# Optimization experiments

Measured on AMD Instinct MI355X. Metric: run time of the kernel, lower is better.

Reference implementation:

```python
import jax, jax.numpy as jnp
import numpy as np

EMB = 1024
HEADS = 16
HEAD_DIM = EMB // HEADS

def setup_inputs() -> dict:
    key = jax.random.key(0)
    ks = jax.random.split(key, 12)
    s = 0.02
    x = jax.random.normal(ks[0], (2, 2048, EMB), dtype=jnp.float32)
    return {
        "x": x,
        "wq": jax.random.normal(ks[1], (EMB, EMB), jnp.float32) * s,
        "bq": jnp.zeros((EMB,), jnp.float32),
        "wk": jax.random.normal(ks[2], (EMB, EMB), jnp.float32) * s,
        "bk": jnp.zeros((EMB,), jnp.float32),
        "wv": jax.random.normal(ks[3], (EMB, EMB), jnp.float32) * s,
        "bv": jnp.zeros((EMB,), jnp.float32),
        "wo": jax.random.normal(ks[4], (EMB, EMB), jnp.float32) * s,
        "bo": jnp.zeros((EMB,), jnp.float32),
        "gamma": jnp.ones((EMB,), jnp.float32),
        "beta": jnp.zeros((EMB,), jnp.float32),
    }

def _layernorm(x, gamma, beta, eps=1e-5):
    mu = jnp.mean(x, axis=-1, keepdims=True)
    var = jnp.mean(jnp.square(x - mu), axis=-1, keepdims=True)
    return (x - mu) * jax.lax.rsqrt(var + eps) * gamma + beta

def reference(x, wq, bq, wk, bk, wv, bv, wo, bo, gamma, beta):
    B, T, D = x.shape
    H, d_k = HEADS, HEAD_DIM
    # Linear(y = x W^T + b), then split heads
    q = (x @ wq.T + bq).reshape(B, T, H, d_k)
    k = (x @ wk.T + bk).reshape(B, T, H, d_k)
    v = (x @ wv.T + bv).reshape(B, T, H, d_k)
    scores = jnp.einsum('bthd,bshd->bhts', q, k) / jnp.sqrt(jnp.float32(d_k))
    attn = jax.nn.softmax(scores, axis=-1)  # dropout is identity in eval mode
    out = jnp.einsum('bhts,bshd->bthd', attn, v).reshape(B, T, D)
    out = out @ wo.T + bo
    return _layernorm(x + out, gamma, beta)
```

## Files before the change

### kernel.cpp

```cpp
#include <hip/hip_runtime.h>
#include <stdint.h>
#include <stddef.h>


typedef __bf16 bf16_t;
typedef bf16_t bf16x8 __attribute__((ext_vector_type(8)));
typedef float f32x16 __attribute__((ext_vector_type(16)));
typedef float f32x2 __attribute__((ext_vector_type(2)));
typedef uint16_t u16x8 __attribute__((ext_vector_type(8)));

#define MFMA32(a, b, c) __builtin_amdgcn_mfma_f32_32x32x16_bf16((a), (b), (c), 0, 0, 0)

__device__ __forceinline__ uint16_t f2bf(float f) {
  __bf16 h = (__bf16)f;
  return *(uint16_t*)&h;
}

__device__ __forceinline__ void gload16(const void* g, void* l) {
  __builtin_amdgcn_global_load_lds((const __attribute__((address_space(1))) void*)g,
                                   (__attribute__((address_space(3))) void*)l,
                                   16, 0, 0);
}

__global__ __launch_bounds__(256) void cvt_all(
    const float* __restrict__ x, const float* __restrict__ wq,
    const float* __restrict__ wk, const float* __restrict__ wv,
    const float* __restrict__ wo, uint16_t* __restrict__ xb,
    uint16_t* __restrict__ wqb, uint16_t* __restrict__ wkb,
    uint16_t* __restrict__ wvb, uint16_t* __restrict__ wob) {
  const int gid = blockIdx.x * 256 + threadIdx.x;
  const float* src; uint16_t* dst; int off;
  if (gid < 1048576) {
    src = x; dst = xb; off = gid;
  } else {
    const int t = gid - 1048576;
    off = t & 262143;
    switch (t >> 18) {
      case 0: src = wq; dst = wqb; break;
      case 1: src = wk; dst = wkb; break;
      case 2: src = wv; dst = wvb; break;
      default: src = wo; dst = wob; break;
    }
  }
  const float4 f = ((const float4*)src)[off];
  uint64_t p = (uint64_t)f2bf(f.x) | ((uint64_t)f2bf(f.y) << 16) |
               ((uint64_t)f2bf(f.z) << 32) | ((uint64_t)f2bf(f.w) << 48);
  ((uint64_t*)dst)[off] = p;
}

template <int MODE>
__device__ __forceinline__ void gemm128(uint16_t* __restrict__ smem,
                                        const uint16_t* __restrict__ A,
                                        const uint16_t* __restrict__ Bt,
                                        const float* __restrict__ bias,
                                        float oscale,
                                        uint16_t* __restrict__ outb,
                                        int m0, int n0) {
  uint16_t* sAp = smem;
  uint16_t* sBp = smem + 8192;
  const int tid = threadIdx.x;
  const int lane = tid & 63, w = tid >> 6;
  const int l31 = lane & 31, half = lane >> 5;
  const int wm = (w >> 1) * 64, wn = (w & 1) * 64;

  const int ch0 = tid, ch1 = tid + 256;
  const int r0 = ch0 >> 2, g0 = (((ch0 & 3) ^ (r0 & 3)) << 3);
  const int r1 = ch1 >> 2, g1 = (((ch1 & 3) ^ (r1 & 3)) << 3);
  const uint16_t* a0 = A + (size_t)(m0 + r0) * 1024 + g0;
  const uint16_t* a1 = A + (size_t)(m0 + r1) * 1024 + g1;
  const uint16_t* b0 = Bt + (size_t)(n0 + r0) * 1024 + g0;
  const uint16_t* b1 = Bt + (size_t)(n0 + r1) * 1024 + g1;

  gload16(a0, &sAp[ch0 * 8]);
  gload16(a1, &sAp[ch1 * 8]);
  gload16(b0, &sBp[ch0 * 8]);
  gload16(b1, &sBp[ch1 * 8]);

  f32x16 acc[2][2] = {};

  for (int kt = 0; kt < 32; ++kt) {
    __syncthreads();
    const int cur = kt & 1;
    if (kt < 31) {
      const int ko = (kt + 1) * 32;
      const int nxt = cur ^ 1;
      gload16(a0 + ko, &sAp[nxt * 4096 + ch0 * 8]);
      gload16(a1 + ko, &sAp[nxt * 4096 + ch1 * 8]);
      gload16(b0 + ko, &sBp[nxt * 4096 + ch0 * 8]);
      gload16(b1 + ko, &sBp[nxt * 4096 + ch1 * 8]);
    }
#pragma unroll
    for (int s = 0; s < 2; ++s) {
      const int c = s * 2 + half;
      bf16x8 af[2], bfr[2];
#pragma unroll
      for (int i = 0; i < 2; ++i) {
        const int arow = wm + i * 32 + l31;
        af[i] = *(const bf16x8*)&sAp[cur * 4096 + arow * 32 + ((c ^ (arow & 3)) << 3)];
      }
#pragma unroll
      for (int j = 0; j < 2; ++j) {
        const int brow = wn + j * 32 + l31;
        bfr[j] = *(const bf16x8*)&sBp[cur * 4096 + brow * 32 + ((c ^ (brow & 3)) << 3)];
      }
#pragma unroll
      for (int i = 0; i < 2; ++i)
#pragma unroll
        for (int j = 0; j < 2; ++j) acc[i][j] = MFMA32(af[i], bfr[j], acc[i][j]);
    }
  }

  if constexpr (MODE == 2) {
    __syncthreads();
    uint16_t* vT = smem;
#pragma unroll
    for (int i = 0; i < 2; ++i)
#pragma unroll
      for (int j = 0; j < 2; ++j) {
        const int nl = wn + j * 32 + l31;
        const float bv = bias[n0 + nl];
#pragma unroll
        for (int g = 0; g < 4; ++g) {
          uint64_t pk = 0;
#pragma unroll
          for (int e = 0; e < 4; ++e)
            pk |= (uint64_t)f2bf(acc[i][j][g * 4 + e] + bv) << (16 * e);
          const int tl = wm + i * 32 + g * 8 + half * 4;
          *(uint64_t*)&vT[nl * 136 + tl] = pk;
        }
      }
    __syncthreads();
    const int bb = m0 >> 11, tblk = m0 & 2047;
    const int h0 = n0 >> 6;
#pragma unroll
    for (int c = 0; c < 8; ++c) {
      const int idx = c * 256 + tid;
      const int nf = idx >> 4, t8 = (idx & 15) * 8;
      const int tb = t8 & ~15;
      const int add4 = (t8 & 8) ? 4 : 0;
      u16x8 v;
#pragma unroll
      for (int e = 0; e < 8; ++e)
        v[e] = vT[nf * 136 + tb + ((e & 3) + ((e >> 2) << 3)) + add4];
      *(u16x8*)&outb[((size_t)(bb * 16 + h0 + (nf >> 6)) * 64 + (nf & 63)) * 2048 +
                     tblk + t8] = v;
    }
    return;
  }

#pragma unroll
  for (int i = 0; i < 2; ++i) {
#pragma unroll
    for (int j = 0; j < 2; ++j) {
      const int gn = n0 + wn + j * 32 + l31;
      const float bv = bias[gn];
#pragma unroll
      for (int reg = 0; reg < 16; ++reg) {
        const int gm = m0 + wm + i * 32 + (reg & 3) + 8 * (reg >> 2) + 4 * half;
        outb[(size_t)gm * 1024 + gn] = f2bf((acc[i][j][reg] + bv) * oscale);
      }
    }
  }
}

__device__ __forceinline__ void gemm64x128(const uint16_t* __restrict__ A,
                                           const uint16_t* __restrict__ Bt,
                                           const float* __restrict__ bias,
                                           float* __restrict__ outf,
                                           int m0, int n0) {
  __shared__ uint16_t sA[2][64 * 32];
  __shared__ uint16_t sB[2][128 * 32];
  const int tid = threadIdx.x;
  const int lane = tid & 63, w = tid >> 6;
  const int l31 = lane & 31, half = lane >> 5;
  const int wm = (w >> 1) * 32, wn = (w & 1) * 64;

  const int ra = tid >> 2, ga = (((tid & 3) ^ (ra & 3)) << 3);
  const int chb0 = tid, chb1 = tid + 256;
  const int rb0 = chb0 >> 2, gb0 = (((chb0 & 3) ^ (rb0 & 3)) << 3);
  const int rb1 = chb1 >> 2, gb1 = (((chb1 & 3) ^ (rb1 & 3)) << 3);
  const uint16_t* a0 = A + (size_t)(m0 + ra) * 1024 + ga;
  const uint16_t* b0 = Bt + (size_t)(n0 + rb0) * 1024 + gb0;
  const uint16_t* b1 = Bt + (size_t)(n0 + rb1) * 1024 + gb1;

  gload16(a0, &sA[0][tid * 8]);
  gload16(b0, &sB[0][chb0 * 8]);
  gload16(b1, &sB[0][chb1 * 8]);

  f32x16 acc[2] = {};

  for (int kt = 0; kt < 32; ++kt) {
    __syncthreads();
    const int cur = kt & 1;
    if (kt < 31) {
      const int ko = (kt + 1) * 32;
      const int nxt = cur ^ 1;
      gload16(a0 + ko, &sA[nxt][tid * 8]);
      gload16(b0 + ko, &sB[nxt][chb0 * 8]);
      gload16(b1 + ko, &sB[nxt][chb1 * 8]);
    }
#pragma unroll
    for (int s = 0; s < 2; ++s) {
      const int c = s * 2 + half;
      const int arow = wm + l31;
      const bf16x8 af =
          *(const bf16x8*)&sA[cur][arow * 32 + ((c ^ (arow & 3)) << 3)];
      bf16x8 bfr[2];
#pragma unroll
      for (int j = 0; j < 2; ++j) {
        const int brow = wn + j * 32 + l31;
        bfr[j] = *(const bf16x8*)&sB[cur][brow * 32 + ((c ^ (brow & 3)) << 3)];
      }
#pragma unroll
      for (int j = 0; j < 2; ++j) acc[j] = MFMA32(af, bfr[j], acc[j]);
    }
  }

#pragma unroll
  for (int j = 0; j < 2; ++j) {
    const int gn = n0 + wn + j * 32 + l31;
    const float bv = bias[gn];
#pragma unroll
    for (int reg = 0; reg < 16; ++reg) {
      const int gm = m0 + wm + (reg & 3) + 8 * (reg >> 2) + 4 * half;
      outf[(size_t)gm * 1024 + gn] = acc[j][reg] + bv;
    }
  }
}

#define QSCALE 0.18033688011112042f

__global__ __launch_bounds__(256) void qkv_gemm(
    const uint16_t* __restrict__ xb, const uint16_t* __restrict__ wqb,
    const uint16_t* __restrict__ wkb, const uint16_t* __restrict__ wvb,
    const float* __restrict__ bq, const float* __restrict__ bk,
    const float* __restrict__ bv, uint16_t* __restrict__ qb,
    uint16_t* __restrict__ kb, uint16_t* __restrict__ vbT) {
  __shared__ __align__(16) uint16_t smem[17408];
  const int disp = blockIdx.x + 8 * blockIdx.y + 256 * blockIdx.z;
  const int xw = disp / 96;
  const int r = disp - xw * 96;
  const int zw = r >> 5, yw = r & 31;
  const int m0 = yw * 128, n0 = xw * 128;
  if (zw == 0)      gemm128<0>(smem, xb, wqb, bq, QSCALE, qb, m0, n0);
  else if (zw == 1) gemm128<0>(smem, xb, wkb, bk, 1.f, kb, m0, n0);
  else              gemm128<2>(smem, xb, wvb, bv, 1.f, vbT, m0, n0);
}

__global__ __launch_bounds__(256) void o_gemm(const uint16_t* __restrict__ ab,
                                              const uint16_t* __restrict__ wob,
                                              const float* __restrict__ bo,
                                              float* __restrict__ y) {
  const int disp = blockIdx.x + 8 * blockIdx.y;
  const int xw = disp >> 6, yw = disp & 63;
  gemm64x128(ab, wob, bo, y, yw * 64, xw * 128);
}


#define QK_CHUNK(accv, mblk_)                                               \
  do {                                                                      \
    const int srow_ = sh * 64 + (mblk_) * 32 + l31;                         \
    _Pragma("unroll") for (int s4_ = 0; s4_ < 4; ++s4_) {                   \
      const int c_ = s4_ * 2 + half;                                        \
      const bf16x8 kk_ =                                                    \
          *(const bf16x8*)&sKc[srow_ * 64 + ((c_ ^ (srow_ & 7)) << 3)];     \
      accv = MFMA32(kk_, qa[s4_], accv);                                    \
    }                                                                       \
  } while (0)

#define EXP_PACK(accv, b0_, b1_)                                            \
  do {                                                                      \
    _Pragma("unroll") for (int r_ = 0; r_ < 8; r_ += 2) {                   \
      const float pa_ = __builtin_amdgcn_exp2f(accv[r_]);                   \
      const float pb_ = __builtin_amdgcn_exp2f(accv[r_ + 1]);               \
      li2 += (f32x2){pa_, pb_};                                             \
      b0_[r_] = (__bf16)pa_;                                                \
      b0_[r_ + 1] = (__bf16)pb_;                                            \
    }                                                                       \
    _Pragma("unroll") for (int r_ = 0; r_ < 8; r_ += 2) {                   \
      const float pa_ = __builtin_amdgcn_exp2f(accv[r_ + 8]);               \
      const float pb_ = __builtin_amdgcn_exp2f(accv[r_ + 9]);               \
      li2 += (f32x2){pa_, pb_};                                             \
      b1_[r_] = (__bf16)pa_;                                                \
      b1_[r_ + 1] = (__bf16)pb_;                                            \
    }                                                                       \
  } while (0)

#define PV_CHUNK(mblk_, b0_, b1_)                                           \
  do {                                                                      \
    _Pragma("unroll") for (int t_ = 0; t_ < 2; ++t_) {                      \
      const bf16x8 bp_ = t_ ? (b1_) : (b0_);                                \
      const int cc_ = sh * 8 + (mblk_) * 4 + t_ * 2 + half;                 \
      _Pragma("unroll") for (int md_ = 0; md_ < 2; ++md_) {                 \
        const int vrow_ = md_ * 32 + l31;                                   \
        const bf16x8 vv_ =                                                  \
            *(const bf16x8*)&sVc[vrow_ * 128 + ((cc_ ^ (vrow_ & 15)) << 3)];\
        acc_o[md_] = MFMA32(vv_, bp_, acc_o[md_]);                          \
      }                                                                     \
    }                                                                       \
  } while (0)

__global__ __launch_bounds__(1024, 4) void attn(const uint16_t* __restrict__ qb,
                                                const uint16_t* __restrict__ kb,
                                                const uint16_t* __restrict__ vbT,
                                                uint16_t* __restrict__ ab) {
  __shared__ __align__(16) uint16_t smem[32768];
  __shared__ float epl2[512];
  uint16_t* sK = smem;
  uint16_t* sV = smem + 16384;
  const int tid = threadIdx.x;
  const int lane = tid & 63, w = tid >> 6;
  const int l31 = lane & 31, half = lane >> 5;
  const int rg = w & 7, sh = w >> 3;
  const int hb = blockIdx.x;
  const int h = hb & 15, b = hb >> 4;
  const int q0 = blockIdx.y * 256;
  const size_t qkbase = (size_t)b * 2048 * 1024 + (size_t)h * 64;
  const size_t vtbase = (size_t)hb * 64 * 2048;

  const int kr0 = tid >> 3, kg0 = (((tid & 7) ^ (kr0 & 7)) << 3);
  const int vr0 = tid >> 4, vg0 = (((tid & 15) ^ (vr0 & 15)) << 3);
  const uint16_t* k0 = kb + qkbase + (size_t)kr0 * 1024 + kg0;
  const uint16_t* v0 = vbT + vtbase + (size_t)vr0 * 2048 + vg0;

  gload16(k0, sK + tid * 8);
  gload16(v0, sV + tid * 8);

  bf16x8 qa[4];
  {
    const uint16_t* qrow =
        qb + qkbase + (size_t)(q0 + rg * 32 + l31) * 1024 + half * 8;
#pragma unroll
    for (int s4 = 0; s4 < 4; ++s4) qa[s4] = *(const bf16x8*)(qrow + s4 * 16);
  }

  f32x16 acc_o[2] = {};
  f32x2 li2 = {0.f, 0.f};

  for (int kt = 0; kt < 16; ++kt) {
    __syncthreads();
    const int cur = kt & 1;
    if (kt < 15) {
      const size_t soK = (size_t)(kt + 1) * 128 * 1024;
      const int soV = (kt + 1) * 128;
      const int nxt = cur ^ 1;
      gload16(k0 + soK, sK + nxt * 8192 + tid * 8);
      gload16(v0 + soV, sV + nxt * 8192 + tid * 8);
    }
    const uint16_t* sKc = sK + cur * 8192;
    const uint16_t* sVc = sV + cur * 8192;

#pragma unroll
    for (int mblk = 0; mblk < 2; ++mblk) {
      f32x16 accs = {};
      QK_CHUNK(accs, mblk);
      bf16x8 bp0, bp1;
      EXP_PACK(accs, bp0, bp1);
      PV_CHUNK(mblk, bp0, bp1);
    }
  }

  float li = li2.x + li2.y;

  __syncthreads();
  float* ep = (float*)smem;
  if (sh == 1) {
#pragma unroll
    for (int md = 0; md < 2; ++md)
#pragma unroll
      for (int reg = 0; reg < 16; ++reg)
        ep[((rg * 2 + md) * 16 + reg) * 64 + lane] = acc_o[md][reg];
    epl2[rg * 64 + lane] = li;
  }
  __syncthreads();
  if (sh == 0) {
#pragma unroll
    for (int md = 0; md < 2; ++md)
#pragma unroll
      for (int reg = 0; reg < 16; ++reg)
        acc_o[md][reg] += ep[((rg * 2 + md) * 16 + reg) * 64 + lane];
    li += epl2[rg * 64 + lane];
    li += __shfl_xor(li, 32);
    const float inv = 1.f / li;
    const int row = q0 + rg * 32 + l31;
    uint16_t* const obase = ab + (size_t)(b * 2048 + row) * 1024 + h * 64;
#pragma unroll
    for (int md = 0; md < 2; ++md)
#pragma unroll
      for (int g = 0; g < 4; ++g) {
        uint64_t pk = 0;
#pragma unroll
        for (int e = 0; e < 4; ++e)
          pk |= (uint64_t)f2bf(acc_o[md][g * 4 + e] * inv) << (16 * e);
        *(uint64_t*)(obase + md * 32 + g * 8 + half * 4) = pk;
      }
  }
}

__global__ __launch_bounds__(256) void resid_ln(const float* __restrict__ x,
                                                const float* __restrict__ y,
                                                const float* __restrict__ gamma,
                                                const float* __restrict__ beta,
                                                float* __restrict__ out) {
  const int row = blockIdx.x, tid = threadIdx.x;
  const size_t base = (size_t)row * 1024 + tid * 4;
  const float4 xv = *(const float4*)(x + base);
  const float4 yv = *(const float4*)(y + base);
  const float a = xv.x + yv.x, b2 = xv.y + yv.y, c = xv.z + yv.z, d = xv.w + yv.w;
  float s = a + b2 + c + d;
#pragma unroll
  for (int o = 1; o < 64; o <<= 1) s += __shfl_xor(s, o);
  __shared__ float red[4];
  const int w = tid >> 6;
  if ((tid & 63) == 0) red[w] = s;
  __syncthreads();
  const float mu = (red[0] + red[1] + red[2] + red[3]) * (1.f / 1024.f);
  const float da = a - mu, db = b2 - mu, dc = c - mu, dd = d - mu;
  float sq = da * da + db * db + dc * dc + dd * dd;
#pragma unroll
  for (int o = 1; o < 64; o <<= 1) sq += __shfl_xor(sq, o);
  __syncthreads();
  if ((tid & 63) == 0) red[w] = sq;
  __syncthreads();
  const float var = (red[0] + red[1] + red[2] + red[3]) * (1.f / 1024.f);
  const float rs = rsqrtf(var + 1e-5f);
  const float4 g = *(const float4*)(gamma + tid * 4);
  const float4 bt = *(const float4*)(beta + tid * 4);
  float4 o4;
  o4.x = da * rs * g.x + bt.x;
  o4.y = db * rs * g.y + bt.y;
  o4.z = dc * rs * g.z + bt.z;
  o4.w = dd * rs * g.w + bt.w;
  *(float4*)(out + base) = o4;
}

extern "C" void kernel_launch(void* const* d_in, const int* in_sizes, int n_in,
                              void* d_out, int out_size, void* d_ws, size_t ws_size,
                              hipStream_t stream) {
  const float* x     = (const float*)d_in[0];
  const float* wq    = (const float*)d_in[1];
  const float* bq    = (const float*)d_in[2];
  const float* wk    = (const float*)d_in[3];
  const float* bk    = (const float*)d_in[4];
  const float* wv    = (const float*)d_in[5];
  const float* bv    = (const float*)d_in[6];
  const float* wo    = (const float*)d_in[7];
  const float* bo    = (const float*)d_in[8];
  const float* gamma = (const float*)d_in[9];
  const float* beta  = (const float*)d_in[10];
  float* out = (float*)d_out;
  char* ws = (char*)d_ws;
  const size_t MB = 1024 * 1024;
  uint16_t* xb  = (uint16_t*)(ws);
  uint16_t* ab  = xb;
  uint16_t* wqb = (uint16_t*)(ws + 8 * MB);
  uint16_t* wkb = (uint16_t*)(ws + 10 * MB);
  uint16_t* wvb = (uint16_t*)(ws + 12 * MB);
  uint16_t* wob = (uint16_t*)(ws + 14 * MB);
  uint16_t* qb  = (uint16_t*)(ws + 16 * MB);
  uint16_t* kb  = (uint16_t*)(ws + 24 * MB);
  uint16_t* vbT = (uint16_t*)(ws + 40 * MB);
  float*    y   = (float*)(ws + 16 * MB);

  cvt_all<<<8192, 256, 0, stream>>>(x, wq, wk, wv, wo, xb, wqb, wkb, wvb, wob);
  qkv_gemm<<<dim3(8, 32, 3), 256, 0, stream>>>(xb, wqb, wkb, wvb, bq, bk, bv, qb, kb, vbT);
  attn<<<dim3(32, 8), 1024, 0, stream>>>(qb, kb, vbT, ab);
  o_gemm<<<dim3(8, 64), 256, 0, stream>>>(ab, wob, bo, y);
  resid_ln<<<4096, 256, 0, stream>>>(x, y, gamma, beta, out);
}
```

Measured before the change: 197.5 us.

## Triple-buffer GEMM LDS tiles with explicit vmcnt waits for deeper prefetch

Measured after the change: 203.4 us. 3.0% more time.

```diff
diff --git a/kernel.cpp b/kernel.cpp
--- a/kernel.cpp
+++ b/kernel.cpp
@@ -57,7 +57,7 @@
                                         uint16_t* __restrict__ outb,
                                         int m0, int n0) {
   uint16_t* sAp = smem;
-  uint16_t* sBp = smem + 8192;
+  uint16_t* sBp = smem + 12288;
   const int tid = threadIdx.x;
   const int lane = tid & 63, w = tid >> 6;
   const int l31 = lane & 31, half = lane >> 5;
@@ -71,24 +71,27 @@
   const uint16_t* b0 = Bt + (size_t)(n0 + r0) * 1024 + g0;
   const uint16_t* b1 = Bt + (size_t)(n0 + r1) * 1024 + g1;
 
-  gload16(a0, &sAp[ch0 * 8]);
-  gload16(a1, &sAp[ch1 * 8]);
-  gload16(b0, &sBp[ch0 * 8]);
-  gload16(b1, &sBp[ch1 * 8]);
+#define QKV_ISSUE(t_)                                                       \
+  do {                                                                      \
+    const int ko_ = (t_) * 32;                                              \
+    const int bs_ = ((t_) % 3) * 4096;                                      \
+    gload16(a0 + ko_, &sAp[bs_ + ch0 * 8]);                                 \
+    gload16(a1 + ko_, &sAp[bs_ + ch1 * 8]);                                 \
+    gload16(b0 + ko_, &sBp[bs_ + ch0 * 8]);                                 \
+    gload16(b1 + ko_, &sBp[bs_ + ch1 * 8]);                                 \
+  } while (0)
+
+  QKV_ISSUE(0);
+  QKV_ISSUE(1);
 
   f32x16 acc[2][2] = {};
 
   for (int kt = 0; kt < 32; ++kt) {
-    __syncthreads();
-    const int cur = kt & 1;
-    if (kt < 31) {
-      const int ko = (kt + 1) * 32;
-      const int nxt = cur ^ 1;
-      gload16(a0 + ko, &sAp[nxt * 4096 + ch0 * 8]);
-      gload16(a1 + ko, &sAp[nxt * 4096 + ch1 * 8]);
-      gload16(b0 + ko, &sBp[nxt * 4096 + ch0 * 8]);
-      gload16(b1 + ko, &sBp[nxt * 4096 + ch1 * 8]);
-    }
+    if (kt < 31) asm volatile("s_waitcnt vmcnt(4)" ::: "memory");
+    else         asm volatile("s_waitcnt vmcnt(0)" ::: "memory");
+    __builtin_amdgcn_s_barrier();
+    if (kt < 30) QKV_ISSUE(kt + 2);
+    const int cur = (kt % 3) * 4096;
 #pragma unroll
     for (int s = 0; s < 2; ++s) {
       const int c = s * 2 + half;
@@ -96,12 +99,12 @@
 #pragma unroll
       for (int i = 0; i < 2; ++i) {
         const int arow = wm + i * 32 + l31;
-        af[i] = *(const bf16x8*)&sAp[cur * 4096 + arow * 32 + ((c ^ (arow & 3)) << 3)];
+        af[i] = *(const bf16x8*)&sAp[cur + arow * 32 + ((c ^ (arow & 3)) << 3)];
       }
 #pragma unroll
       for (int j = 0; j < 2; ++j) {
         const int brow = wn + j * 32 + l31;
-        bfr[j] = *(const bf16x8*)&sBp[cur * 4096 + brow * 32 + ((c ^ (brow & 3)) << 3)];
+        bfr[j] = *(const bf16x8*)&sBp[cur + brow * 32 + ((c ^ (brow & 3)) << 3)];
       }
 #pragma unroll
       for (int i = 0; i < 2; ++i)
@@ -109,6 +112,7 @@
         for (int j = 0; j < 2; ++j) acc[i][j] = MFMA32(af[i], bfr[j], acc[i][j]);
     }
   }
+#undef QKV_ISSUE
 
   if constexpr (MODE == 2) {
     __syncthreads();
@@ -168,8 +172,8 @@
                                            const float* __restrict__ bias,
                                            float* __restrict__ outf,
                                            int m0, int n0) {
-  __shared__ uint16_t sA[2][64 * 32];
-  __shared__ uint16_t sB[2][128 * 32];
+  __shared__ uint16_t sA[3][64 * 32];
+  __shared__ uint16_t sB[3][128 * 32];
   const int tid = threadIdx.x;
   const int lane = tid & 63, w = tid >> 6;
   const int l31 = lane & 31, half = lane >> 5;
@@ -183,22 +187,26 @@
   const uint16_t* b0 = Bt + (size_t)(n0 + rb0) * 1024 + gb0;
   const uint16_t* b1 = Bt + (size_t)(n0 + rb1) * 1024 + gb1;
 
-  gload16(a0, &sA[0][tid * 8]);
-  gload16(b0, &sB[0][chb0 * 8]);
-  gload16(b1, &sB[0][chb1 * 8]);
+#define O_ISSUE(t_)                                                         \
+  do {                                                                      \
+    const int ko_ = (t_) * 32;                                              \
+    const int bs_ = (t_) % 3;                                               \
+    gload16(a0 + ko_, &sA[bs_][tid * 8]);                                   \
+    gload16(b0 + ko_, &sB[bs_][chb0 * 8]);                                  \
+    gload16(b1 + ko_, &sB[bs_][chb1 * 8]);                                  \
+  } while (0)
+
+  O_ISSUE(0);
+  O_ISSUE(1);
 
   f32x16 acc[2] = {};
 
   for (int kt = 0; kt < 32; ++kt) {
-    __syncthreads();
-    const int cur = kt & 1;
-    if (kt < 31) {
-      const int ko = (kt + 1) * 32;
-      const int nxt = cur ^ 1;
-      gload16(a0 + ko, &sA[nxt][tid * 8]);
-      gload16(b0 + ko, &sB[nxt][chb0 * 8]);
-      gload16(b1 + ko, &sB[nxt][chb1 * 8]);
-    }
+    if (kt < 31) asm volatile("s_waitcnt vmcnt(3)" ::: "memory");
+    else         asm volatile("s_waitcnt vmcnt(0)" ::: "memory");
+    __builtin_amdgcn_s_barrier();
+    if (kt < 30) O_ISSUE(kt + 2);
+    const int cur = kt % 3;
 #pragma unroll
     for (int s = 0; s < 2; ++s) {
       const int c = s * 2 + half;
@@ -215,6 +223,7 @@
       for (int j = 0; j < 2; ++j) acc[j] = MFMA32(af, bfr[j], acc[j]);
     }
   }
+#undef O_ISSUE
 
 #pragma unroll
   for (int j = 0; j < 2; ++j) {
@@ -236,7 +245,7 @@
     const float* __restrict__ bq, const float* __restrict__ bk,
     const float* __restrict__ bv, uint16_t* __restrict__ qb,
     uint16_t* __restrict__ kb, uint16_t* __restrict__ vbT) {
-  __shared__ __align__(16) uint16_t smem[17408];
+  __shared__ __align__(16) uint16_t smem[24576];
   const int disp = blockIdx.x + 8 * blockIdx.y + 256 * blockIdx.z;
   const int xw = disp / 96;
   const int r = disp - xw * 96;
```
